# Kernel tuning notes

Hardware: AMD Instinct MI355X
Metric: run time of the kernel (lower is better)

## Reference

```python
import jax, jax.numpy as jnp
import numpy as np

B, S, H, C = 2, 160, 768, 5  # batch, seq_len, bert hidden, num_case(4)+coref(1)


def setup_inputs() -> dict:
    key = jax.random.key(0)
    ks = jax.random.split(key, 8)
    sequence_output = jax.random.normal(ks[0], (B, S, H), jnp.float32)
    w_prd = jax.random.normal(ks[1], (H, C * H), jnp.float32) * 0.02
    b_prd = jnp.zeros((C * H,), jnp.float32)
    w_arg = jax.random.normal(ks[2], (H, C * H), jnp.float32) * 0.02
    b_arg = jnp.zeros((C * H,), jnp.float32)
    w_out = jax.random.normal(ks[3], (H,), jnp.float32) * 0.02
    mask = jax.random.randint(ks[4], (B, S, C, S), 0, 2).astype(bool)
    target = jax.random.randint(ks[5], (B, S, C, S), 0, 2).astype(jnp.int32)
    return {
        "sequence_output": sequence_output,
        "w_prd": w_prd, "b_prd": b_prd,
        "w_arg": w_arg, "b_arg": b_arg,
        "w_out": w_out,
        "mask": mask, "target": target,
    }


def reference(sequence_output, w_prd, b_prd, w_arg, b_arg, w_out, mask, target):
    b, s, h = sequence_output.shape
    c = b_prd.shape[0] // h
    # Linear projections, reshaped to per-case views: [B, S, C, H]
    h_p = (sequence_output @ w_prd + b_prd).reshape(b, s, c, h)
    h_a = (sequence_output @ w_arg + b_arg).reshape(b, s, c, h)
    # Broadcast-add over predicate/argument positions: [B, Sp, Sa, C, H]
    # (dropout is identity in eval; dropout=0.0)
    h_pa = jnp.tanh(h_p[:, :, None, :, :] + h_a[:, None, :, :, :])
    # Rank-1 reduction over hidden (nn.Linear(H, 1, bias=False)): [B, Sp, Sa, C]
    scores = jnp.einsum("bpach,h->bpac", h_pa, w_out)
    # transpose(2, 3): [B, Sp, C, Sa]
    scores = jnp.transpose(scores, (0, 1, 3, 2))
    output = scores + (~mask).astype(scores.dtype) * -1024.0
    # cross_entropy_pas_loss: softmax over argument axis, summed over gold labels
    log_sm = jax.nn.log_softmax(output, axis=3)
    t = target.astype(output.dtype)
    loss = jnp.sum(-log_sm * t) / (jnp.sum(t) + 1e-6)
    return loss, output
```

## Files before the change

kernel.cpp:

```cpp
#include <hip/hip_runtime.h>
#include <hip/hip_bf16.h>
#include <math.h>


typedef __attribute__((ext_vector_type(8))) short bf16x8;
typedef __attribute__((ext_vector_type(4))) float f32x4;

__device__ __forceinline__ unsigned short f2bf(float f) {
    union { float f; unsigned u; } v; v.f = f;
    unsigned r = (v.u + 0x7FFFu + ((v.u >> 16) & 1u)) >> 16;
    return (unsigned short)r;
}

__device__ __forceinline__ unsigned pack2bf(float lo, float hi) {
    union { float f; unsigned u; } a, b; a.f = lo; b.f = hi;
    return ((a.u + 0x8000u) >> 16) | ((b.u + 0x8000u) & 0xFFFF0000u);
}

__global__ __launch_bounds__(256) void convert_bf16(
    const float* __restrict__ A,
    const float* __restrict__ Wp,
    const float* __restrict__ Wa,
    unsigned short* __restrict__ A_bf,
    unsigned short* __restrict__ Wp_bf,
    unsigned short* __restrict__ Wa_bf)
{
    const int NA = 320 * 768 / 8;
    const int NW = 768 * 3840 / 8;
    int i = blockIdx.x * 256 + threadIdx.x;
    const float* src; unsigned short* dst; int off;
    if (i < NA)            { src = A;  dst = A_bf;  off = i; }
    else if (i < NA + NW)  { src = Wp; dst = Wp_bf; off = i - NA; }
    else                   { src = Wa; dst = Wa_bf; off = i - NA - NW; }
    float4 v0 = *reinterpret_cast<const float4*>(src + (size_t)off * 8);
    float4 v1 = *reinterpret_cast<const float4*>(src + (size_t)off * 8 + 4);
    bf16x8 o;
    o[0] = f2bf(v0.x); o[1] = f2bf(v0.y); o[2] = f2bf(v0.z); o[3] = f2bf(v0.w);
    o[4] = f2bf(v1.x); o[5] = f2bf(v1.y); o[6] = f2bf(v1.z); o[7] = f2bf(v1.w);
    *reinterpret_cast<bf16x8*>(dst + (size_t)off * 8) = o;
}

__global__ __launch_bounds__(256) void proj_gemm_bf16(
    const unsigned short* __restrict__ A_bf,
    const unsigned short* __restrict__ Wp_bf,
    const float* __restrict__ bp,
    const unsigned short* __restrict__ Wa_bf,
    const float* __restrict__ ba,
    float* __restrict__ hp,
    float* __restrict__ ha)
{
    const int which = blockIdx.z;
    const unsigned short* W = which ? Wa_bf : Wp_bf;
    const float* bias       = which ? ba : bp;
    float* out              = which ? ha : hp;

    const int n0 = blockIdx.x * 64;
    const int m0 = blockIdx.y * 64;
    const int tid  = threadIdx.x;
    const int lane = tid & 63;
    const int w    = tid >> 6;

    __shared__ __attribute__((aligned(16))) unsigned short As[64][72];
    __shared__ __attribute__((aligned(16))) unsigned short Bs[64][72];

    f32x4 acc[2][2] = {};

    const int am = tid >> 2;
    const int ak = (tid & 3) * 16;
    const unsigned short* Arow = A_bf + (size_t)(m0 + am) * 768 + ak;

    const int nb = tid & 63;
    const int kt = (tid >> 6) * 16;
    const unsigned short* Wbase = W + (size_t)kt * 3840 + n0 + nb;

    const int wm = (w & 1) * 32;
    const int wn = (w >> 1) * 32;
    const int fr = lane & 15;
    const int fk = (lane >> 4) * 8;

    for (int k0 = 0; k0 < 768; k0 += 64) {
        bf16x8 a0 = *reinterpret_cast<const bf16x8*>(Arow + k0);
        bf16x8 a1 = *reinterpret_cast<const bf16x8*>(Arow + k0 + 8);
        unsigned short bv[16];
        const unsigned short* wp = Wbase + (size_t)k0 * 3840;
        #pragma unroll
        for (int j = 0; j < 16; ++j) bv[j] = wp[(size_t)j * 3840];

        __syncthreads();

        *reinterpret_cast<bf16x8*>(&As[am][ak])     = a0;
        *reinterpret_cast<bf16x8*>(&As[am][ak + 8]) = a1;
        bf16x8 b0, b1;
        #pragma unroll
        for (int j = 0; j < 8; ++j) { b0[j] = (short)bv[j]; b1[j] = (short)bv[8 + j]; }
        *reinterpret_cast<bf16x8*>(&Bs[nb][kt])     = b0;
        *reinterpret_cast<bf16x8*>(&Bs[nb][kt + 8]) = b1;

        __syncthreads();

        #pragma unroll
        for (int kk = 0; kk < 2; ++kk) {
            const int kc = kk * 32 + fk;
            bf16x8 af0 = *reinterpret_cast<const bf16x8*>(&As[wm + fr][kc]);
            bf16x8 af1 = *reinterpret_cast<const bf16x8*>(&As[wm + 16 + fr][kc]);
            bf16x8 bg0 = *reinterpret_cast<const bf16x8*>(&Bs[wn + fr][kc]);
            bf16x8 bg1 = *reinterpret_cast<const bf16x8*>(&Bs[wn + 16 + fr][kc]);
            acc[0][0] = __builtin_amdgcn_mfma_f32_16x16x32_bf16(af0, bg0, acc[0][0], 0, 0, 0);
            acc[0][1] = __builtin_amdgcn_mfma_f32_16x16x32_bf16(af0, bg1, acc[0][1], 0, 0, 0);
            acc[1][0] = __builtin_amdgcn_mfma_f32_16x16x32_bf16(af1, bg0, acc[1][0], 0, 0, 0);
            acc[1][1] = __builtin_amdgcn_mfma_f32_16x16x32_bf16(af1, bg1, acc[1][1], 0, 0, 0);
        }
    }

    #pragma unroll
    for (int j = 0; j < 2; ++j) {
        const int col = n0 + wn + j * 16 + fr;
        const float bb = bias[col];
        #pragma unroll
        for (int i = 0; i < 2; ++i) {
            #pragma unroll
            for (int r = 0; r < 4; ++r) {
                const int row = m0 + wm + i * 16 + (lane >> 4) * 4 + r;
                float t = tanhf(acc[i][j][r] + bb);
                t = __builtin_amdgcn_fmed3f(t, -0.999999f, 0.999999f);
                out[(size_t)row * 3840 + col] = t;
            }
        }
    }
}

__global__ __launch_bounds__(64) void scores_mfma(
    const float* __restrict__ tp_g,
    const float* __restrict__ ta_g,
    const float* __restrict__ w_out,
    float* __restrict__ part_s)
{
    const int at0 = blockIdx.x * 32;
    const int pt0 = blockIdx.y * 32;
    const int z   = blockIdx.z;
    const int bc  = z >> 3;
    const int hq  = z & 7;
    const int b = bc / 5, c = bc % 5;

    const int lane = threadIdx.x;
    const int r    = lane >> 1;
    const int hh   = (lane & 1) * 16;
    const int fr   = lane & 15;
    const int fk   = (lane >> 4) * 8;

    __shared__ __attribute__((aligned(16))) unsigned short Pb[2][32][40];
    __shared__ __attribute__((aligned(16))) unsigned short Gb[2][32][40];

    f32x4 acc[2][2] = {};

    const float* psrc = tp_g + (size_t)(b * 160 + pt0 + r) * 3840 + c * 768 + hq * 96 + hh;
    const float* asrc = ta_g + (size_t)(b * 160 + at0 + r) * 3840 + c * 768 + hq * 96 + hh;
    const float* wsrc = w_out + hq * 96 + hh;

    for (int ch = 0; ch < 3; ++ch) {
        float tp[16], nta[16], pw[16], gc[16], g1[16];
        {
            float tav[16], wv[16];
#define LD16(arr, ptr) { \
            float4 v_; \
            v_ = *reinterpret_cast<const float4*>((ptr));      arr[0]=v_.x; arr[1]=v_.y; arr[2]=v_.z; arr[3]=v_.w; \
            v_ = *reinterpret_cast<const float4*>((ptr) + 4);  arr[4]=v_.x; arr[5]=v_.y; arr[6]=v_.z; arr[7]=v_.w; \
            v_ = *reinterpret_cast<const float4*>((ptr) + 8);  arr[8]=v_.x; arr[9]=v_.y; arr[10]=v_.z; arr[11]=v_.w; \
            v_ = *reinterpret_cast<const float4*>((ptr) + 12); arr[12]=v_.x; arr[13]=v_.y; arr[14]=v_.z; arr[15]=v_.w; }
            LD16(tp,  psrc + ch * 32)
            LD16(tav, asrc + ch * 32)
            LD16(wv,  wsrc + ch * 32)
#undef LD16
            #pragma unroll
            for (int e = 0; e < 16; ++e) {
                float ta_ = tav[e];
                gc[e]  = wv[e] * ta_;
                g1[e]  = wv[e] * fmaf(-ta_, ta_, 1.f);
                nta[e] = -ta_;
                pw[e]  = 1.0f;
            }
        }

        #pragma unroll
        for (int j = 0; j < 8; ++j) {
            const int pp = j & 1;
            uint4 q;
            q.x = pack2bf(pw[0],  pw[1]);  q.y = pack2bf(pw[2],  pw[3]);
            q.z = pack2bf(pw[4],  pw[5]);  q.w = pack2bf(pw[6],  pw[7]);
            *reinterpret_cast<uint4*>(&Pb[pp][r][hh]) = q;
            q.x = pack2bf(pw[8],  pw[9]);  q.y = pack2bf(pw[10], pw[11]);
            q.z = pack2bf(pw[12], pw[13]); q.w = pack2bf(pw[14], pw[15]);
            *reinterpret_cast<uint4*>(&Pb[pp][r][hh + 8]) = q;
            q.x = pack2bf(gc[0],  gc[1]);  q.y = pack2bf(gc[2],  gc[3]);
            q.z = pack2bf(gc[4],  gc[5]);  q.w = pack2bf(gc[6],  gc[7]);
            *reinterpret_cast<uint4*>(&Gb[pp][r][hh]) = q;
            q.x = pack2bf(gc[8],  gc[9]);  q.y = pack2bf(gc[10], gc[11]);
            q.z = pack2bf(gc[12], gc[13]); q.w = pack2bf(gc[14], gc[15]);
            *reinterpret_cast<uint4*>(&Gb[pp][r][hh + 8]) = q;

            bf16x8 af0 = *reinterpret_cast<const bf16x8*>(&Pb[pp][fr][fk]);
            bf16x8 af1 = *reinterpret_cast<const bf16x8*>(&Pb[pp][16 + fr][fk]);
            bf16x8 bg0 = *reinterpret_cast<const bf16x8*>(&Gb[pp][fr][fk]);
            bf16x8 bg1 = *reinterpret_cast<const bf16x8*>(&Gb[pp][16 + fr][fk]);
            acc[0][0] = __builtin_amdgcn_mfma_f32_16x16x32_bf16(af0, bg0, acc[0][0], 0, 0, 0);
            acc[0][1] = __builtin_amdgcn_mfma_f32_16x16x32_bf16(af0, bg1, acc[0][1], 0, 0, 0);
            acc[1][0] = __builtin_amdgcn_mfma_f32_16x16x32_bf16(af1, bg0, acc[1][0], 0, 0, 0);
            acc[1][1] = __builtin_amdgcn_mfma_f32_16x16x32_bf16(af1, bg1, acc[1][1], 0, 0, 0);

            #pragma unroll
            for (int e = 0; e < 16; ++e) {
                pw[e] *= tp[e];
                gc[e] = (j == 0) ? g1[e] : gc[e] * nta[e];
            }
        }
    }

    float* dst = part_s + (size_t)hq * 256000;
    #pragma unroll
    for (int i = 0; i < 2; ++i) {
        #pragma unroll
        for (int jj = 0; jj < 2; ++jj) {
            #pragma unroll
            for (int rr = 0; rr < 4; ++rr) {
                const int p = pt0 + i * 16 + (lane >> 4) * 4 + rr;
                const int a = at0 + jj * 16 + fr;
                dst[((size_t)(b * 160 + p) * 5 + c) * 160 + a] = acc[i][jj][rr];
            }
        }
    }
}

__global__ __launch_bounds__(256) void loss_kernel(
    const float* __restrict__ part_s,
    const int*  __restrict__ mask,
    const int*  __restrict__ target,
    float* __restrict__ scores_out,
    float* __restrict__ part)
{
    const int lane = threadIdx.x & 63;
    const int wid  = threadIdx.x >> 6;
    const int row  = blockIdx.x * 4 + wid;
    const size_t base = (size_t)row * 160;

    float x0 = 0.f, x1 = 0.f, x2 = 0.f;
    #pragma unroll
    for (int k = 0; k < 8; ++k) {
        const float* ps = part_s + (size_t)k * 256000 + base;
        x0 += ps[lane];
        x1 += ps[lane + 64];
        if (lane < 32) x2 += ps[lane + 128];
    }
    x0 += mask[base + lane] ? 0.f : -1024.f;
    x1 += mask[base + lane + 64] ? 0.f : -1024.f;
    if (lane < 32) x2 += mask[base + lane + 128] ? 0.f : -1024.f;

    scores_out[base + lane] = x0;
    scores_out[base + lane + 64] = x1;
    if (lane < 32) scores_out[base + lane + 128] = x2;

    float x2r = (lane < 32) ? x2 : -INFINITY;

    float m = fmaxf(fmaxf(x0, x1), x2r);
    #pragma unroll
    for (int o = 32; o >= 1; o >>= 1)
        m = fmaxf(m, __shfl_xor(m, o));

    float s = __expf(x0 - m) + __expf(x1 - m) + ((lane < 32) ? __expf(x2 - m) : 0.f);
    #pragma unroll
    for (int o = 32; o >= 1; o >>= 1)
        s += __shfl_xor(s, o);
    float lse = logf(s) + m;

    const int* t = target + base;
    int t0 = t[lane], t1 = t[lane + 64];
    int t2 = (lane < 32) ? t[lane + 128] : 0;
    float pl = (float)t0 * (lse - x0) + (float)t1 * (lse - x1)
             + ((lane < 32 && t2) ? (float)t2 * (lse - x2) : 0.f);
    float pts = (float)(t0 + t1 + t2);
    #pragma unroll
    for (int o = 32; o >= 1; o >>= 1) {
        pl  += __shfl_xor(pl, o);
        pts += __shfl_xor(pts, o);
    }

    __shared__ float sp[4], st[4];
    if (lane == 0) { sp[wid] = pl; st[wid] = pts; }
    __syncthreads();
    if (threadIdx.x == 0) {
        part[blockIdx.x * 2]     = sp[0] + sp[1] + sp[2] + sp[3];
        part[blockIdx.x * 2 + 1] = st[0] + st[1] + st[2] + st[3];
    }
}

__global__ __launch_bounds__(256) void finalize_kernel(
    const float* __restrict__ part, float* __restrict__ out0)
{
    const int tid = threadIdx.x;
    float pl = 0.f, pts = 0.f;
    for (int i = tid; i < 400; i += 256) {
        pl  += part[i * 2];
        pts += part[i * 2 + 1];
    }
    #pragma unroll
    for (int o = 32; o >= 1; o >>= 1) {
        pl  += __shfl_xor(pl, o);
        pts += __shfl_xor(pts, o);
    }
    __shared__ float sp[4], st[4];
    const int wid = tid >> 6;
    if ((tid & 63) == 0) { sp[wid] = pl; st[wid] = pts; }
    __syncthreads();
    if (tid == 0) {
        float tl = sp[0] + sp[1] + sp[2] + sp[3];
        float tt = st[0] + st[1] + st[2] + st[3];
        out0[0] = tl / (tt + 1e-6f);
    }
}

extern "C" void kernel_launch(void* const* d_in, const int* in_sizes, int n_in,
                              void* d_out, int out_size, void* d_ws, size_t ws_size,
                              hipStream_t stream) {
    const float* seq   = (const float*)d_in[0];
    const float* w_prd = (const float*)d_in[1];
    const float* b_prd = (const float*)d_in[2];
    const float* w_arg = (const float*)d_in[3];
    const float* b_arg = (const float*)d_in[4];
    const float* w_out = (const float*)d_in[5];
    const int*   mask  = (const int*)d_in[6];
    const int*   targ  = (const int*)d_in[7];

    float* out = (float*)d_out;

    char* ws = (char*)d_ws;
    float* hp     = (float*)ws;
    float* ha     = (float*)(ws + 4915200);
    float* part_s = (float*)(ws + 9830400);
    float* part   = (float*)(ws + 18022400);
    unsigned short* A_bf  = (unsigned short*)(ws + 18025600);
    unsigned short* Wp_bf = (unsigned short*)(ws + 18517120);
    unsigned short* Wa_bf = (unsigned short*)(ws + 24415360);

    convert_bf16<<<3000, 256, 0, stream>>>(seq, w_prd, w_arg, A_bf, Wp_bf, Wa_bf);

    dim3 g1(60, 5, 2);
    proj_gemm_bf16<<<g1, 256, 0, stream>>>(A_bf, Wp_bf, b_prd, Wa_bf, b_arg, hp, ha);

    dim3 g2(5, 5, 80);
    scores_mfma<<<g2, 64, 0, stream>>>(hp, ha, w_out, part_s);

    loss_kernel<<<400, 256, 0, stream>>>(part_s, mask, targ, out + 1, part);
    finalize_kernel<<<1, 256, 0, stream>>>(part, out);
}
```

Baseline: 50.72 us.

## Build MFMA operands directly in registers instead of staging through LDS

Each lane now loads the exact rows and k-slice it needs for the MFMA fragment layout, computes the power-series terms in registers, and packs them straight into bf16 operands. This removes the LDS write/read round trip (and its implicit wave-level hazards) for every MFMA step. In exchange each lane loads and computes two rows' worth of values (duplicating elementwise work across the lanes that share a row) and uses more registers.

Result: no change. 51.57 us (+1.7%).

```diff
diff --git a/kernel.cpp b/kernel.cpp
--- a/kernel.cpp
+++ b/kernel.cpp
@@ -15,6 +15,13 @@
 __device__ __forceinline__ unsigned pack2bf(float lo, float hi) {
     union { float f; unsigned u; } a, b; a.f = lo; b.f = hi;
     return ((a.u + 0x8000u) >> 16) | ((b.u + 0x8000u) & 0xFFFF0000u);
+}
+
+__device__ __forceinline__ bf16x8 pack8(const float* v) {
+    union { uint4 q; bf16x8 h; } u;
+    u.q.x = pack2bf(v[0], v[1]); u.q.y = pack2bf(v[2], v[3]);
+    u.q.z = pack2bf(v[4], v[5]); u.q.w = pack2bf(v[6], v[7]);
+    return u.h;
 }
 
 __global__ __launch_bounds__(256) void convert_bf16(
@@ -143,77 +150,68 @@
     const int b = bc / 5, c = bc % 5;
 
     const int lane = threadIdx.x;
-    const int r    = lane >> 1;
-    const int hh   = (lane & 1) * 16;
     const int fr   = lane & 15;
-    const int fk   = (lane >> 4) * 8;
-
-    __shared__ __attribute__((aligned(16))) unsigned short Pb[2][32][40];
-    __shared__ __attribute__((aligned(16))) unsigned short Gb[2][32][40];
+    const int fk8  = (lane >> 4) * 8;
 
     f32x4 acc[2][2] = {};
 
-    const float* psrc = tp_g + (size_t)(b * 160 + pt0 + r) * 3840 + c * 768 + hq * 96 + hh;
-    const float* asrc = ta_g + (size_t)(b * 160 + at0 + r) * 3840 + c * 768 + hq * 96 + hh;
-    const float* wsrc = w_out + hq * 96 + hh;
+    const size_t koff = c * 768 + hq * 96 + fk8;
+    const float* prow0 = tp_g + (size_t)(b * 160 + pt0 + fr) * 3840 + koff;
+    const float* prow1 = prow0 + (size_t)16 * 3840;
+    const float* arow0 = ta_g + (size_t)(b * 160 + at0 + fr) * 3840 + koff;
+    const float* arow1 = arow0 + (size_t)16 * 3840;
+    const float* wptr  = w_out + hq * 96 + fk8;
+
+#define LD8(arr, ptr) { \
+    float4 v_ = *reinterpret_cast<const float4*>(ptr); \
+    arr[0]=v_.x; arr[1]=v_.y; arr[2]=v_.z; arr[3]=v_.w; \
+    v_ = *reinterpret_cast<const float4*>((ptr) + 4); \
+    arr[4]=v_.x; arr[5]=v_.y; arr[6]=v_.z; arr[7]=v_.w; }
 
     for (int ch = 0; ch < 3; ++ch) {
-        float tp[16], nta[16], pw[16], gc[16], g1[16];
+        float tpv[2][8], pw[2][8], gc[2][8], g1v[2][8], ntav[2][8];
         {
-            float tav[16], wv[16];
-#define LD16(arr, ptr) { \
-            float4 v_; \
-            v_ = *reinterpret_cast<const float4*>((ptr));      arr[0]=v_.x; arr[1]=v_.y; arr[2]=v_.z; arr[3]=v_.w; \
-            v_ = *reinterpret_cast<const float4*>((ptr) + 4);  arr[4]=v_.x; arr[5]=v_.y; arr[6]=v_.z; arr[7]=v_.w; \
-            v_ = *reinterpret_cast<const float4*>((ptr) + 8);  arr[8]=v_.x; arr[9]=v_.y; arr[10]=v_.z; arr[11]=v_.w; \
-            v_ = *reinterpret_cast<const float4*>((ptr) + 12); arr[12]=v_.x; arr[13]=v_.y; arr[14]=v_.z; arr[15]=v_.w; }
-            LD16(tp,  psrc + ch * 32)
-            LD16(tav, asrc + ch * 32)
-            LD16(wv,  wsrc + ch * 32)
-#undef LD16
+            float tav0[8], tav1[8], wv[8];
+            LD8(tpv[0], prow0 + ch * 32)
+            LD8(tpv[1], prow1 + ch * 32)
+            LD8(tav0,   arow0 + ch * 32)
+            LD8(tav1,   arow1 + ch * 32)
+            LD8(wv,     wptr  + ch * 32)
             #pragma unroll
-            for (int e = 0; e < 16; ++e) {
-                float ta_ = tav[e];
-                gc[e]  = wv[e] * ta_;
-                g1[e]  = wv[e] * fmaf(-ta_, ta_, 1.f);
-                nta[e] = -ta_;
-                pw[e]  = 1.0f;
+            for (int e = 0; e < 8; ++e) {
+                gc[0][e]   = wv[e] * tav0[e];
+                gc[1][e]   = wv[e] * tav1[e];
+                g1v[0][e]  = wv[e] * fmaf(-tav0[e], tav0[e], 1.f);
+                g1v[1][e]  = wv[e] * fmaf(-tav1[e], tav1[e], 1.f);
+                ntav[0][e] = -tav0[e];
+                ntav[1][e] = -tav1[e];
+                pw[0][e] = 1.0f;
+                pw[1][e] = 1.0f;
             }
         }
 
         #pragma unroll
         for (int j = 0; j < 8; ++j) {
-            const int pp = j & 1;
-            uint4 q;
-            q.x = pack2bf(pw[0],  pw[1]);  q.y = pack2bf(pw[2],  pw[3]);
-            q.z = pack2bf(pw[4],  pw[5]);  q.w = pack2bf(pw[6],  pw[7]);
-            *reinterpret_cast<uint4*>(&Pb[pp][r][hh]) = q;
-            q.x = pack2bf(pw[8],  pw[9]);  q.y = pack2bf(pw[10], pw[11]);
-            q.z = pack2bf(pw[12], pw[13]); q.w = pack2bf(pw[14], pw[15]);
-            *reinterpret_cast<uint4*>(&Pb[pp][r][hh + 8]) = q;
-            q.x = pack2bf(gc[0],  gc[1]);  q.y = pack2bf(gc[2],  gc[3]);
-            q.z = pack2bf(gc[4],  gc[5]);  q.w = pack2bf(gc[6],  gc[7]);
-            *reinterpret_cast<uint4*>(&Gb[pp][r][hh]) = q;
-            q.x = pack2bf(gc[8],  gc[9]);  q.y = pack2bf(gc[10], gc[11]);
-            q.z = pack2bf(gc[12], gc[13]); q.w = pack2bf(gc[14], gc[15]);
-            *reinterpret_cast<uint4*>(&Gb[pp][r][hh + 8]) = q;
-
-            bf16x8 af0 = *reinterpret_cast<const bf16x8*>(&Pb[pp][fr][fk]);
-            bf16x8 af1 = *reinterpret_cast<const bf16x8*>(&Pb[pp][16 + fr][fk]);
-            bf16x8 bg0 = *reinterpret_cast<const bf16x8*>(&Gb[pp][fr][fk]);
-            bf16x8 bg1 = *reinterpret_cast<const bf16x8*>(&Gb[pp][16 + fr][fk]);
+            bf16x8 af0 = pack8(pw[0]);
+            bf16x8 af1 = pack8(pw[1]);
+            bf16x8 bg0 = pack8(gc[0]);
+            bf16x8 bg1 = pack8(gc[1]);
             acc[0][0] = __builtin_amdgcn_mfma_f32_16x16x32_bf16(af0, bg0, acc[0][0], 0, 0, 0);
             acc[0][1] = __builtin_amdgcn_mfma_f32_16x16x32_bf16(af0, bg1, acc[0][1], 0, 0, 0);
             acc[1][0] = __builtin_amdgcn_mfma_f32_16x16x32_bf16(af1, bg0, acc[1][0], 0, 0, 0);
             acc[1][1] = __builtin_amdgcn_mfma_f32_16x16x32_bf16(af1, bg1, acc[1][1], 0, 0, 0);
-
-            #pragma unroll
-            for (int e = 0; e < 16; ++e) {
-                pw[e] *= tp[e];
-                gc[e] = (j == 0) ? g1[e] : gc[e] * nta[e];
+            if (j < 7) {
+                #pragma unroll
+                for (int e = 0; e < 8; ++e) {
+                    pw[0][e] *= tpv[0][e];
+                    pw[1][e] *= tpv[1][e];
+                    gc[0][e] = (j == 0) ? g1v[0][e] : gc[0][e] * ntav[0][e];
+                    gc[1][e] = (j == 0) ? g1v[1][e] : gc[1][e] * ntav[1][e];
+                }
             }
         }
     }
+#undef LD8
 
     float* dst = part_s + (size_t)hq * 256000;
     #pragma unroll
```
